# Performance work log

Measured on AMD Instinct MI355X. Metric: run time of the kernel, lower is better.

Reference implementation:

```python
import jax, jax.numpy as jnp
import numpy as np

B, S, D_IN, D_OUT = 8, 2048, 1024, 1024

def setup_inputs() -> dict:
    key = jax.random.key(0)
    ks = jax.random.split(key, 6)
    return {
        "inputs_for_keys": jax.random.normal(ks[0], (B, S, D_IN), dtype=jnp.float32),
        "inputs_for_values": jax.random.normal(ks[1], (B, S, D_IN), dtype=jnp.float32),
        "inputs_for_queries": jax.random.normal(ks[2], (B, S, D_IN), dtype=jnp.float32),
        "W_K": jax.random.normal(ks[3], (D_IN, D_OUT), dtype=jnp.float32) * 0.05,
        "W_V": jax.random.normal(ks[4], (D_IN, D_OUT), dtype=jnp.float32) * 0.05,
        "W_Q": jax.random.normal(ks[5], (D_IN, D_OUT), dtype=jnp.float32) * 0.05,
    }

def reference(inputs_for_keys, inputs_for_values, inputs_for_queries, W_K, W_V, W_Q):
    # Linear projections: [B,S,D_in] @ [D_in,D_out] -> [B,S,D_out]
    K = jnp.einsum("bsd,de->bse", inputs_for_keys, W_K)
    V = jnp.einsum("bsd,de->bse", inputs_for_values, W_V)
    Q = jnp.einsum("bsd,de->bse", inputs_for_queries, W_Q)
    scale = jnp.sqrt(jnp.asarray(K.shape[-1], dtype=K.dtype))
    # Scaled dot-product attention scores: [B,Sq,Sk]
    scores = jnp.einsum("bqe,bke->bqk", Q, K) / scale
    probs = jax.nn.softmax(scores, axis=-1)
    Z = jnp.einsum("bqk,bke->bqe", probs, V)
    return Z
```

## Files before the change

kernel.cpp:

```cpp
#include <hip/hip_runtime.h>
#include <hip/hip_bf16.h>
#include <stdint.h>

#define BATCH 8
#define SEQ 2048
#define DMODEL 1024

typedef __attribute__((ext_vector_type(4))) float f32x4;
typedef __attribute__((ext_vector_type(8))) short bf16x8;
typedef __attribute__((ext_vector_type(4))) uint32_t u32x4;
typedef __attribute__((ext_vector_type(2))) uint32_t u32x2;

#define MFMA16(a, b, c) __builtin_amdgcn_mfma_f32_16x16x32_bf16((a), (b), (c), 0, 0, 0)


static __device__ __forceinline__ uint16_t f2bf(float f) {
    uint32_t u = __builtin_bit_cast(uint32_t, f);
    u += 0x7fffu + ((u >> 16) & 1u);
    return (uint16_t)(u >> 16);
}
static __device__ __forceinline__ uint32_t pk2(float lo, float hi) {
    return (uint32_t)f2bf(lo) | ((uint32_t)f2bf(hi) << 16);
}
static __device__ __forceinline__ void gload16(const uint16_t* g, uint16_t* l) {
    __builtin_amdgcn_global_load_lds((const __attribute__((address_space(1))) void*)g,
                                     (__attribute__((address_space(3))) void*)l, 16, 0, 0);
}

__global__ __launch_bounds__(256) void cast_bf16_pk(const float* __restrict__ src,
                                                    uint16_t* __restrict__ dst) {
    const size_t c = (size_t)blockIdx.x * 256 + threadIdx.x;
    const size_t panel = c >> 11;
    const int w = (int)(c & 2047);
    const int ks = w >> 4, r15 = w & 15;
    const float* s = src + (panel * 16 + r15) * DMODEL + ks * 8;
    f32x4 a = *(const f32x4*)s;
    f32x4 b = *(const f32x4*)(s + 4);
    u32x4 o = {pk2(a[0], a[1]), pk2(a[2], a[3]), pk2(b[0], b[1]), pk2(b[2], b[3])};
    *(u32x4*)(dst + c * 8) = o;
}

__global__ void wt_cast_kernel(const float* __restrict__ Wk, const float* __restrict__ Wv,
                               const float* __restrict__ Wq, uint16_t* __restrict__ WT) {
    const float* W = blockIdx.z == 0 ? Wk : (blockIdx.z == 1 ? Wv : Wq);
    uint16_t* dst = WT + (size_t)blockIdx.z * DMODEL * DMODEL;
    __shared__ float tile[32][33];
    const int x = blockIdx.x * 32, y = blockIdx.y * 32;
    const int tx = threadIdx.x, ty = threadIdx.y;
#pragma unroll
    for (int j = 0; j < 4; j++)
        tile[ty * 4 + j][tx] = W[(size_t)(y + ty * 4 + j) * DMODEL + x + tx];
    __syncthreads();
#pragma unroll
    for (int j = 0; j < 4; j++) {
        const int n = x + ty * 4 + j, k = y + tx;
        const size_t off = ((size_t)(n >> 4) * (DMODEL / 8) + (k >> 3)) * 128 +
                           (n & 15) * 8 + (k & 7);
        dst[off] = f2bf(tile[tx][ty * 4 + j]);
    }
}

#define STAGE(tile, s)                                        \
    do {                                                      \
        const size_t ko_ = (size_t)(tile) * 512;              \
        gload16(Ab + ko_ + abase0, &As[s][t * 8]);            \
        gload16(Ab + ko_ + abase1, &As[s][t * 8 + 4096]);     \
        gload16(Bb + ko_ + bbase0, &Bs[s][t * 8]);            \
        gload16(Bb + ko_ + bbase1, &Bs[s][t * 8 + 4096]);     \
    } while (0)

#define KBODY(s, WAITSTR)                                                              \
    do {                                                                               \
        asm volatile("s_waitcnt " WAITSTR ::: "memory");                               \
        __builtin_amdgcn_s_barrier();                                                  \
        bf16x8 bfr[4], afr[8];                                                         \
        _Pragma("unroll") for (int j = 0; j < 4; j++)                                  \
            bfr[j] = *(const bf16x8*)&Bs[s][(wc * 4 + j) * 512 + lg * 128 + lr * 8];   \
        _Pragma("unroll") for (int i = 0; i < 8; i++)                                  \
            afr[i] = *(const bf16x8*)&As[s][(wr * 8 + i) * 512 + lg * 128 + lr * 8];   \
        __builtin_amdgcn_s_setprio(1);                                                 \
        _Pragma("unroll") for (int i = 0; i < 4; i++)                                  \
            _Pragma("unroll") for (int j = 0; j < 4; j++)                              \
                acc[i][j] = MFMA16(afr[i], bfr[j], acc[i][j]);                         \
        __builtin_amdgcn_s_setprio(0);                                                 \
        __builtin_amdgcn_s_setprio(1);                                                 \
        _Pragma("unroll") for (int i = 4; i < 8; i++)                                  \
            _Pragma("unroll") for (int j = 0; j < 4; j++)                              \
                acc[i][j] = MFMA16(afr[i], bfr[j], acc[i][j]);                         \
        __builtin_amdgcn_s_setprio(0);                                                 \
        asm volatile("s_waitcnt lgkmcnt(0)" ::: "memory");                             \
        __builtin_amdgcn_sched_barrier(0);                                             \
        __builtin_amdgcn_s_barrier();                                                  \
    } while (0)

template <int MODE, int BX>
__global__ __launch_bounds__(512, 2) void gemm256(const uint16_t* __restrict__ Ag,
                                                  const uint16_t* __restrict__ Bg,
                                                  void* __restrict__ Cg,
                                                  const float* __restrict__ Linv,
                                                  float scale, int lda, int ldb, int ldc,
                                                  int nk, size_t sA, size_t sB, size_t sC) {
    __shared__ __align__(16) uint16_t As[3][256 * 32];
    __shared__ __align__(16) uint16_t Bs[3][256 * 32];
    const int bz = BX ? blockIdx.x : blockIdx.z;
    const int bm = BX ? blockIdx.y : blockIdx.x;
    const int bn = BX ? blockIdx.z : blockIdx.y;
    const int m0 = bm * 256, n0 = bn * 256;
    const uint16_t* Ab = Ag + (size_t)bz * sA + (size_t)m0 * lda;
    const uint16_t* Bb = Bg + (size_t)bz * sB + (size_t)n0 * ldb;
    const int t = threadIdx.x, lane = t & 63;
    const int wid = t >> 6, wr = wid >> 2, wc = wid & 3;
    const int lr = lane & 15, lg = lane >> 4;
    const size_t eldA = (size_t)lda * 16, eldB = (size_t)ldb * 16;
    const size_t abase0 = (size_t)(t >> 6) * eldA + (t & 63) * 8;
    const size_t abase1 = abase0 + 8 * eldA;
    const size_t bbase0 = (size_t)(t >> 6) * eldB + (t & 63) * 8;
    const size_t bbase1 = bbase0 + 8 * eldB;

    f32x4 acc[8][4] = {};
    STAGE(0, 0);
    STAGE(1, 1);
    int s = 0, s2 = 2;
    for (int kt = 0; kt < nk - 2; ++kt) {
        STAGE(kt + 2, s2);
        KBODY(s, "vmcnt(8)");
        s = (s == 2) ? 0 : s + 1;
        s2 = (s2 == 2) ? 0 : s2 + 1;
    }
    KBODY(s, "vmcnt(4)");
    s = (s == 2) ? 0 : s + 1;
    KBODY(s, "vmcnt(0)");

    if constexpr (MODE == 0) {
        uint16_t* C = (uint16_t*)Cg + (size_t)bz * sC;
#pragma unroll
        for (int i = 0; i < 8; i++) {
            const int gm = m0 + wr * 128 + i * 16 + lg * 4;
            const size_t pbase = (size_t)(gm >> 4) * (ldc / 8);
#pragma unroll
            for (int j = 0; j < 4; j++) {
                const int gn = n0 + wc * 64 + j * 16 + lr;
                const size_t off = (pbase + (gn >> 3)) * 128 + (gn & 7);
#pragma unroll
                for (int r = 0; r < 4; r++)
                    C[off + (lg * 4 + r) * 8] = f2bf(acc[i][j][r] * scale);
            }
        }
    } else if constexpr (MODE == 1) {
        uint16_t* C = (uint16_t*)Cg;
#pragma unroll
        for (int i = 0; i < 8; i++) {
            const int gm = m0 + wr * 128 + i * 16 + lg * 4;
            const int bb = gm / SEQ;
            const int s0 = gm - bb * SEQ;
            uint16_t* Cb = C + (size_t)bb * DMODEL * SEQ;
#pragma unroll
            for (int j = 0; j < 4; j++) {
                const int e = n0 + wc * 64 + j * 16 + lr;
                const size_t off = ((size_t)(e >> 4) * (SEQ / 8) + (s0 >> 3)) * 128 +
                                   (e & 15) * 8 + (s0 & 7);
                u32x2 v = {pk2(acc[i][j][0], acc[i][j][1]), pk2(acc[i][j][2], acc[i][j][3])};
                *(u32x2*)&Cb[off] = v;
            }
        }
    } else {
        float* C = (float*)Cg + (size_t)bz * sC;
        const float* LB = Linv + bz * SEQ;
#pragma unroll
        for (int i = 0; i < 8; i++) {
            const int gm = m0 + wr * 128 + i * 16 + lg * 4;
            const f32x4 lv = *(const f32x4*)&LB[gm];
#pragma unroll
            for (int j = 0; j < 4; j++) {
                const int gn = n0 + wc * 64 + j * 16 + lr;
#pragma unroll
                for (int r = 0; r < 4; r++)
                    C[(size_t)(gm + r) * ldc + gn] = acc[i][j][r] * lv[r];
            }
        }
    }
}

__global__ __launch_bounds__(256) void softmax_pk(uint16_t* __restrict__ S,
                                                  float* __restrict__ Linv) {
    const size_t panel = blockIdx.x;
    uint16_t* sp = S + panel * (size_t)(16 * SEQ);
    const int t = threadIdx.x, lane = t & 63, w = t >> 6;
    const int r15 = t & 15, ksl = t >> 4;
    __shared__ float rm[4][16], rs[4][16];
    u32x4 raw[16];
    float mx = -3.0e38f;
#pragma unroll
    for (int u = 0; u < 16; u++) {
        raw[u] = *(const u32x4*)&sp[(ksl + u * 16) * 128 + r15 * 8];
#pragma unroll
        for (int j = 0; j < 4; j++) {
            mx = fmaxf(mx, __builtin_bit_cast(float, raw[u][j] << 16));
            mx = fmaxf(mx, __builtin_bit_cast(float, raw[u][j] & 0xffff0000u));
        }
    }
    mx = fmaxf(mx, __shfl_xor(mx, 16));
    mx = fmaxf(mx, __shfl_xor(mx, 32));
    if (lane < 16) rm[w][lane] = mx;
    __syncthreads();
    const float m = fmaxf(fmaxf(rm[0][r15], rm[1][r15]), fmaxf(rm[2][r15], rm[3][r15]));
    float sum = 0.0f;
#pragma unroll
    for (int u = 0; u < 16; u++) {
#pragma unroll
        for (int j = 0; j < 4; j++) {
            float lo = __expf(__builtin_bit_cast(float, raw[u][j] << 16) - m);
            float hi = __expf(__builtin_bit_cast(float, raw[u][j] & 0xffff0000u) - m);
            sum += lo + hi;
            raw[u][j] = pk2(lo, hi);
        }
    }
    sum += __shfl_xor(sum, 16);
    sum += __shfl_xor(sum, 32);
    if (lane < 16) rs[w][lane] = sum;
    __syncthreads();
    const float tot = rs[0][r15] + rs[1][r15] + rs[2][r15] + rs[3][r15];
#pragma unroll
    for (int u = 0; u < 16; u++)
        *(u32x4*)&sp[(ksl + u * 16) * 128 + r15 * 8] = raw[u];
    if (w == 0 && lane < 16) Linv[panel * 16 + lane] = 1.0f / tot;
}

extern "C" void kernel_launch(void* const* d_in, const int* in_sizes, int n_in,
                              void* d_out, int out_size, void* d_ws, size_t ws_size,
                              hipStream_t stream) {
    const float* Xk = (const float*)d_in[0];
    const float* Xv = (const float*)d_in[1];
    const float* Xq = (const float*)d_in[2];
    const float* Wk = (const float*)d_in[3];
    const float* Wv = (const float*)d_in[4];
    const float* Wq = (const float*)d_in[5];
    float* out = (float*)d_out;
    char* ws = (char*)d_ws;
    uint16_t* Qbf = (uint16_t*)(ws);
    uint16_t* Kbf = (uint16_t*)(ws + (size_t)33554432);
    uint16_t* VTb = (uint16_t*)(ws + (size_t)67108864);
    uint16_t* WT  = (uint16_t*)(ws + (size_t)100663296);
    float*    Linv= (float*)(ws + (size_t)106954752);
    uint16_t* Sb  = (uint16_t*)(ws + (size_t)107020288);
    uint16_t* Xbf = (uint16_t*)(ws + (size_t)171966464);

    wt_cast_kernel<<<dim3(32, 32, 3), dim3(32, 8), 0, stream>>>(Wk, Wv, Wq, WT);
    cast_bf16_pk<<<8192, 256, 0, stream>>>(Xq, Xbf);
    gemm256<0, 0><<<dim3(64, 4, 1), 512, 0, stream>>>(
        Xbf, WT + 2 * 1048576, (void*)Qbf, nullptr, 0.03125f,
        DMODEL, DMODEL, DMODEL, DMODEL / 32, 0, 0, 0);
    cast_bf16_pk<<<8192, 256, 0, stream>>>(Xk, Xbf);
    gemm256<0, 0><<<dim3(64, 4, 1), 512, 0, stream>>>(
        Xbf, WT, (void*)Kbf, nullptr, 1.0f,
        DMODEL, DMODEL, DMODEL, DMODEL / 32, 0, 0, 0);
    cast_bf16_pk<<<8192, 256, 0, stream>>>(Xv, Xbf);
    gemm256<1, 0><<<dim3(64, 4, 1), 512, 0, stream>>>(
        Xbf, WT + 1048576, (void*)VTb, nullptr, 1.0f,
        DMODEL, DMODEL, 0, DMODEL / 32, 0, 0, 0);
    gemm256<0, 1><<<dim3(8, 8, 8), 512, 0, stream>>>(
        Qbf, Kbf, (void*)Sb, nullptr, 1.0f,
        DMODEL, DMODEL, SEQ, DMODEL / 32,
        (size_t)SEQ * DMODEL, (size_t)SEQ * DMODEL, (size_t)SEQ * SEQ);
    softmax_pk<<<dim3(BATCH * SEQ / 16), 256, 0, stream>>>(Sb, Linv);
    gemm256<2, 1><<<dim3(8, 8, 4), 512, 0, stream>>>(
        Sb, VTb, (void*)out, Linv, 1.0f,
        SEQ, SEQ, DMODEL, SEQ / 32,
        (size_t)SEQ * SEQ, (size_t)DMODEL * SEQ, (size_t)SEQ * DMODEL);
}
```

Measured before the change: 405.7 us.

## Parameterize GEMM N-tile width and switch to double-buffered LDS pipeline

```diff
diff --git a/kernel.cpp b/kernel.cpp
--- a/kernel.cpp
+++ b/kernel.cpp
@@ -60,32 +60,33 @@
     }
 }
 
-#define STAGE(tile, s)                                        \
-    do {                                                      \
-        const size_t ko_ = (size_t)(tile) * 512;              \
-        gload16(Ab + ko_ + abase0, &As[s][t * 8]);            \
-        gload16(Ab + ko_ + abase1, &As[s][t * 8 + 4096]);     \
-        gload16(Bb + ko_ + bbase0, &Bs[s][t * 8]);            \
-        gload16(Bb + ko_ + bbase1, &Bs[s][t * 8 + 4096]);     \
+#define STAGE(tile, s)                                                       \
+    do {                                                                     \
+        const size_t ko_ = (size_t)(tile) * 512;                             \
+        gload16(Ab + ko_ + abase0, &As[s][t * 8]);                           \
+        gload16(Ab + ko_ + abase1, &As[s][t * 8 + 4096]);                    \
+        gload16(Bb + ko_ + bbase0, &Bs[s][t * 8]);                           \
+        if constexpr (NB == 4)                                               \
+            gload16(Bb + ko_ + bbase1, &Bs[s][t * 8 + 4096]);                \
     } while (0)
 
 #define KBODY(s, WAITSTR)                                                              \
     do {                                                                               \
         asm volatile("s_waitcnt " WAITSTR ::: "memory");                               \
         __builtin_amdgcn_s_barrier();                                                  \
-        bf16x8 bfr[4], afr[8];                                                         \
-        _Pragma("unroll") for (int j = 0; j < 4; j++)                                  \
-            bfr[j] = *(const bf16x8*)&Bs[s][(wc * 4 + j) * 512 + lg * 128 + lr * 8];   \
+        bf16x8 bfr[NB], afr[8];                                                        \
+        _Pragma("unroll") for (int j = 0; j < NB; j++)                                 \
+            bfr[j] = *(const bf16x8*)&Bs[s][(wc * NB + j) * 512 + lg * 128 + lr * 8];  \
         _Pragma("unroll") for (int i = 0; i < 8; i++)                                  \
             afr[i] = *(const bf16x8*)&As[s][(wr * 8 + i) * 512 + lg * 128 + lr * 8];   \
         __builtin_amdgcn_s_setprio(1);                                                 \
         _Pragma("unroll") for (int i = 0; i < 4; i++)                                  \
-            _Pragma("unroll") for (int j = 0; j < 4; j++)                              \
+            _Pragma("unroll") for (int j = 0; j < NB; j++)                             \
                 acc[i][j] = MFMA16(afr[i], bfr[j], acc[i][j]);                         \
         __builtin_amdgcn_s_setprio(0);                                                 \
         __builtin_amdgcn_s_setprio(1);                                                 \
         _Pragma("unroll") for (int i = 4; i < 8; i++)                                  \
-            _Pragma("unroll") for (int j = 0; j < 4; j++)                              \
+            _Pragma("unroll") for (int j = 0; j < NB; j++)                             \
                 acc[i][j] = MFMA16(afr[i], bfr[j], acc[i][j]);                         \
         __builtin_amdgcn_s_setprio(0);                                                 \
         asm volatile("s_waitcnt lgkmcnt(0)" ::: "memory");                             \
@@ -93,19 +94,19 @@
         __builtin_amdgcn_s_barrier();                                                  \
     } while (0)
 
-template <int MODE, int BX>
+template <int MODE, int BX, int NB>
 __global__ __launch_bounds__(512, 2) void gemm256(const uint16_t* __restrict__ Ag,
                                                   const uint16_t* __restrict__ Bg,
                                                   void* __restrict__ Cg,
                                                   const float* __restrict__ Linv,
                                                   float scale, int lda, int ldb, int ldc,
                                                   int nk, size_t sA, size_t sB, size_t sC) {
-    __shared__ __align__(16) uint16_t As[3][256 * 32];
-    __shared__ __align__(16) uint16_t Bs[3][256 * 32];
+    __shared__ __align__(16) uint16_t As[2][256 * 32];
+    __shared__ __align__(16) uint16_t Bs[2][NB * 64 * 32];
     const int bz = BX ? blockIdx.x : blockIdx.z;
     const int bm = BX ? blockIdx.y : blockIdx.x;
     const int bn = BX ? blockIdx.z : blockIdx.y;
-    const int m0 = bm * 256, n0 = bn * 256;
+    const int m0 = bm * 256, n0 = bn * (NB * 64);
     const uint16_t* Ab = Ag + (size_t)bz * sA + (size_t)m0 * lda;
     const uint16_t* Bb = Bg + (size_t)bz * sB + (size_t)n0 * ldb;
     const int t = threadIdx.x, lane = t & 63;
@@ -117,19 +118,19 @@
     const size_t bbase0 = (size_t)(t >> 6) * eldB + (t & 63) * 8;
     const size_t bbase1 = bbase0 + 8 * eldB;
 
-    f32x4 acc[8][4] = {};
+    f32x4 acc[8][NB] = {};
     STAGE(0, 0);
-    STAGE(1, 1);
-    int s = 0, s2 = 2;
-    for (int kt = 0; kt < nk - 2; ++kt) {
-        STAGE(kt + 2, s2);
-        KBODY(s, "vmcnt(8)");
-        s = (s == 2) ? 0 : s + 1;
-        s2 = (s2 == 2) ? 0 : s2 + 1;
-    }
-    KBODY(s, "vmcnt(4)");
-    s = (s == 2) ? 0 : s + 1;
-    KBODY(s, "vmcnt(0)");
+    int buf = 0;
+    for (int kt = 0; kt < nk; ++kt) {
+        if (kt + 1 < nk) {
+            STAGE(kt + 1, buf ^ 1);
+            if constexpr (NB == 4) { KBODY(buf, "vmcnt(4)"); }
+            else                   { KBODY(buf, "vmcnt(3)"); }
+        } else {
+            KBODY(buf, "vmcnt(0)");
+        }
+        buf ^= 1;
+    }
 
     if constexpr (MODE == 0) {
         uint16_t* C = (uint16_t*)Cg + (size_t)bz * sC;
@@ -138,8 +139,8 @@
             const int gm = m0 + wr * 128 + i * 16 + lg * 4;
             const size_t pbase = (size_t)(gm >> 4) * (ldc / 8);
 #pragma unroll
-            for (int j = 0; j < 4; j++) {
-                const int gn = n0 + wc * 64 + j * 16 + lr;
+            for (int j = 0; j < NB; j++) {
+                const int gn = n0 + wc * (NB * 16) + j * 16 + lr;
                 const size_t off = (pbase + (gn >> 3)) * 128 + (gn & 7);
 #pragma unroll
                 for (int r = 0; r < 4; r++)
@@ -155,8 +156,8 @@
             const int s0 = gm - bb * SEQ;
             uint16_t* Cb = C + (size_t)bb * DMODEL * SEQ;
 #pragma unroll
-            for (int j = 0; j < 4; j++) {
-                const int e = n0 + wc * 64 + j * 16 + lr;
+            for (int j = 0; j < NB; j++) {
+                const int e = n0 + wc * (NB * 16) + j * 16 + lr;
                 const size_t off = ((size_t)(e >> 4) * (SEQ / 8) + (s0 >> 3)) * 128 +
                                    (e & 15) * 8 + (s0 & 7);
                 u32x2 v = {pk2(acc[i][j][0], acc[i][j][1]), pk2(acc[i][j][2], acc[i][j][3])};
@@ -171,8 +172,8 @@
             const int gm = m0 + wr * 128 + i * 16 + lg * 4;
             const f32x4 lv = *(const f32x4*)&LB[gm];
 #pragma unroll
-            for (int j = 0; j < 4; j++) {
-                const int gn = n0 + wc * 64 + j * 16 + lr;
+            for (int j = 0; j < NB; j++) {
+                const int gn = n0 + wc * (NB * 16) + j * 16 + lr;
 #pragma unroll
                 for (int r = 0; r < 4; r++)
                     C[(size_t)(gm + r) * ldc + gn] = acc[i][j][r] * lv[r];
@@ -247,23 +248,23 @@
 
     wt_cast_kernel<<<dim3(32, 32, 3), dim3(32, 8), 0, stream>>>(Wk, Wv, Wq, WT);
     cast_bf16_pk<<<8192, 256, 0, stream>>>(Xq, Xbf);
-    gemm256<0, 0><<<dim3(64, 4, 1), 512, 0, stream>>>(
+    gemm256<0, 0, 2><<<dim3(64, 8, 1), 512, 0, stream>>>(
         Xbf, WT + 2 * 1048576, (void*)Qbf, nullptr, 0.03125f,
         DMODEL, DMODEL, DMODEL, DMODEL / 32, 0, 0, 0);
     cast_bf16_pk<<<8192, 256, 0, stream>>>(Xk, Xbf);
-    gemm256<0, 0><<<dim3(64, 4, 1), 512, 0, stream>>>(
+    gemm256<0, 0, 2><<<dim3(64, 8, 1), 512, 0, stream>>>(
         Xbf, WT, (void*)Kbf, nullptr, 1.0f,
         DMODEL, DMODEL, DMODEL, DMODEL / 32, 0, 0, 0);
     cast_bf16_pk<<<8192, 256, 0, stream>>>(Xv, Xbf);
-    gemm256<1, 0><<<dim3(64, 4, 1), 512, 0, stream>>>(
+    gemm256<1, 0, 2><<<dim3(64, 8, 1), 512, 0, stream>>>(
         Xbf, WT + 1048576, (void*)VTb, nullptr, 1.0f,
         DMODEL, DMODEL, 0, DMODEL / 32, 0, 0, 0);
-    gemm256<0, 1><<<dim3(8, 8, 8), 512, 0, stream>>>(
+    gemm256<0, 1, 4><<<dim3(8, 8, 8), 512, 0, stream>>>(
         Qbf, Kbf, (void*)Sb, nullptr, 1.0f,
         DMODEL, DMODEL, SEQ, DMODEL / 32,
         (size_t)SEQ * DMODEL, (size_t)SEQ * DMODEL, (size_t)SEQ * SEQ);
     softmax_pk<<<dim3(BATCH * SEQ / 16), 256, 0, stream>>>(Sb, Linv);
-    gemm256<2, 1><<<dim3(8, 8, 4), 512, 0, stream>>>(
+    gemm256<2, 1, 2><<<dim3(8, 8, 8), 512, 0, stream>>>(
         Sb, VTb, (void*)out, Linv, 1.0f,
         SEQ, SEQ, DMODEL, SEQ / 32,
         (size_t)SEQ * SEQ, (size_t)DMODEL * SEQ, (size_t)SEQ * DMODEL);
```

New measurement: 825.3 us. 103% more time.

## Restructure GEMM main loop into 8-phase ping-pong with 64-wide K tiles

Applied to the files above, without the earlier changes.

```diff
diff --git a/kernel.cpp b/kernel.cpp
--- a/kernel.cpp
+++ b/kernel.cpp
@@ -60,76 +60,105 @@
     }
 }
 
-#define STAGE(tile, s)                                        \
-    do {                                                      \
-        const size_t ko_ = (size_t)(tile) * 512;              \
-        gload16(Ab + ko_ + abase0, &As[s][t * 8]);            \
-        gload16(Ab + ko_ + abase1, &As[s][t * 8 + 4096]);     \
-        gload16(Bb + ko_ + bbase0, &Bs[s][t * 8]);            \
-        gload16(Bb + ko_ + bbase1, &Bs[s][t * 8 + 4096]);     \
+#define STG_A(kt, sl, h)                                                          \
+    do {                                                                          \
+        const size_t g0 = (size_t)((h) * 8 + (tid >> 7)) * eldA +                 \
+                          (size_t)(kt) * 1024 + (tid & 127) * 8;                  \
+        gload16(Ab + g0, &As[sl][(h) * 8192 + tid * 8]);                          \
+        gload16(Ab + g0 + 4 * eldA, &As[sl][(h) * 8192 + tid * 8 + 4096]);        \
     } while (0)
-
-#define KBODY(s, WAITSTR)                                                              \
-    do {                                                                               \
-        asm volatile("s_waitcnt " WAITSTR ::: "memory");                               \
-        __builtin_amdgcn_s_barrier();                                                  \
-        bf16x8 bfr[4], afr[8];                                                         \
-        _Pragma("unroll") for (int j = 0; j < 4; j++)                                  \
-            bfr[j] = *(const bf16x8*)&Bs[s][(wc * 4 + j) * 512 + lg * 128 + lr * 8];   \
-        _Pragma("unroll") for (int i = 0; i < 8; i++)                                  \
-            afr[i] = *(const bf16x8*)&As[s][(wr * 8 + i) * 512 + lg * 128 + lr * 8];   \
-        __builtin_amdgcn_s_setprio(1);                                                 \
-        _Pragma("unroll") for (int i = 0; i < 4; i++)                                  \
-            _Pragma("unroll") for (int j = 0; j < 4; j++)                              \
-                acc[i][j] = MFMA16(afr[i], bfr[j], acc[i][j]);                         \
-        __builtin_amdgcn_s_setprio(0);                                                 \
-        __builtin_amdgcn_s_setprio(1);                                                 \
-        _Pragma("unroll") for (int i = 4; i < 8; i++)                                  \
-            _Pragma("unroll") for (int j = 0; j < 4; j++)                              \
-                acc[i][j] = MFMA16(afr[i], bfr[j], acc[i][j]);                         \
-        __builtin_amdgcn_s_setprio(0);                                                 \
-        asm volatile("s_waitcnt lgkmcnt(0)" ::: "memory");                             \
-        __builtin_amdgcn_sched_barrier(0);                                             \
-        __builtin_amdgcn_s_barrier();                                                  \
+#define STG_B(kt, sl, h)                                                          \
+    do {                                                                          \
+        const size_t g0 = (size_t)((h) * 8 + (tid >> 7)) * eldB +                 \
+                          (size_t)(kt) * 1024 + (tid & 127) * 8;                  \
+        gload16(Bb + g0, &Bs[sl][(h) * 8192 + tid * 8]);                          \
+        gload16(Bb + g0 + 4 * eldB, &Bs[sl][(h) * 8192 + tid * 8 + 4096]);        \
     } while (0)
 
+#define READ_B(sl)                                                                \
+    _Pragma("unroll") for (int j = 0; j < 4; j++) {                               \
+        bfr[j][0] = *(const bf16x8*)&Bs[sl][(wc * 4 + j) * 1024 + lbase];         \
+        bfr[j][1] = *(const bf16x8*)&Bs[sl][(wc * 4 + j) * 1024 + 512 + lbase];   \
+    }
+
+#define VM4 asm volatile("s_waitcnt vmcnt(4)" ::: "memory")
+#define VM0 asm volatile("s_waitcnt vmcnt(0)" ::: "memory")
+#define NOPW (void)0
+#define NOST (void)0
+
+#define PH(sl, q, STG, WAIT)                                                      \
+    do {                                                                          \
+        const int ab = (wr * 8 + 2 * (q)) * 1024 + lbase;                         \
+        bf16x8 a00 = *(const bf16x8*)&As[sl][ab];                                 \
+        bf16x8 a01 = *(const bf16x8*)&As[sl][ab + 512];                           \
+        bf16x8 a10 = *(const bf16x8*)&As[sl][ab + 1024];                          \
+        bf16x8 a11 = *(const bf16x8*)&As[sl][ab + 1536];                          \
+        STG;                                                                      \
+        WAIT;                                                                     \
+        __builtin_amdgcn_s_barrier();                                             \
+        asm volatile("s_waitcnt lgkmcnt(0)" ::: "memory");                        \
+        __builtin_amdgcn_sched_barrier(0);                                        \
+        __builtin_amdgcn_s_setprio(1);                                            \
+        _Pragma("unroll") for (int j = 0; j < 4; j++) {                           \
+            acc[2 * (q)][j] = MFMA16(a00, bfr[j][0], acc[2 * (q)][j]);            \
+            acc[2 * (q)][j] = MFMA16(a01, bfr[j][1], acc[2 * (q)][j]);            \
+            acc[2 * (q) + 1][j] = MFMA16(a10, bfr[j][0], acc[2 * (q) + 1][j]);    \
+            acc[2 * (q) + 1][j] = MFMA16(a11, bfr[j][1], acc[2 * (q) + 1][j]);    \
+        }                                                                         \
+        __builtin_amdgcn_s_setprio(0);                                            \
+        __builtin_amdgcn_s_barrier();                                             \
+    } while (0)
+
 template <int MODE, int BX>
-__global__ __launch_bounds__(512, 2) void gemm256(const uint16_t* __restrict__ Ag,
-                                                  const uint16_t* __restrict__ Bg,
-                                                  void* __restrict__ Cg,
-                                                  const float* __restrict__ Linv,
-                                                  float scale, int lda, int ldb, int ldc,
-                                                  int nk, size_t sA, size_t sB, size_t sC) {
-    __shared__ __align__(16) uint16_t As[3][256 * 32];
-    __shared__ __align__(16) uint16_t Bs[3][256 * 32];
+__global__ __launch_bounds__(512, 2) void gemm8p(const uint16_t* __restrict__ Ag,
+                                                 const uint16_t* __restrict__ Bg,
+                                                 void* __restrict__ Cg,
+                                                 const float* __restrict__ Linv,
+                                                 float scale, int lda, int ldb, int ldc,
+                                                 int nk, size_t sA, size_t sB, size_t sC) {
+    __shared__ __align__(16) uint16_t As[2][16384];
+    __shared__ __align__(16) uint16_t Bs[2][16384];
     const int bz = BX ? blockIdx.x : blockIdx.z;
     const int bm = BX ? blockIdx.y : blockIdx.x;
     const int bn = BX ? blockIdx.z : blockIdx.y;
     const int m0 = bm * 256, n0 = bn * 256;
     const uint16_t* Ab = Ag + (size_t)bz * sA + (size_t)m0 * lda;
     const uint16_t* Bb = Bg + (size_t)bz * sB + (size_t)n0 * ldb;
-    const int t = threadIdx.x, lane = t & 63;
-    const int wid = t >> 6, wr = wid >> 2, wc = wid & 3;
+    const int tid = threadIdx.x, lane = tid & 63;
+    const int wid = tid >> 6, wr = wid >> 2, wc = wid & 3;
     const int lr = lane & 15, lg = lane >> 4;
+    const int lbase = lg * 128 + lr * 8;
     const size_t eldA = (size_t)lda * 16, eldB = (size_t)ldb * 16;
-    const size_t abase0 = (size_t)(t >> 6) * eldA + (t & 63) * 8;
-    const size_t abase1 = abase0 + 8 * eldA;
-    const size_t bbase0 = (size_t)(t >> 6) * eldB + (t & 63) * 8;
-    const size_t bbase1 = bbase0 + 8 * eldB;
 
     f32x4 acc[8][4] = {};
-    STAGE(0, 0);
-    STAGE(1, 1);
-    int s = 0, s2 = 2;
-    for (int kt = 0; kt < nk - 2; ++kt) {
-        STAGE(kt + 2, s2);
-        KBODY(s, "vmcnt(8)");
-        s = (s == 2) ? 0 : s + 1;
-        s2 = (s2 == 2) ? 0 : s2 + 1;
-    }
-    KBODY(s, "vmcnt(4)");
-    s = (s == 2) ? 0 : s + 1;
-    KBODY(s, "vmcnt(0)");
+    bf16x8 bfr[4][2];
+    STG_A(0, 0, 0); STG_A(0, 0, 1);
+    STG_B(0, 0, 0); STG_B(0, 0, 1);
+    STG_B(1, 1, 0); STG_B(1, 1, 1);
+    VM4;
+    __builtin_amdgcn_s_barrier();
+    for (int kt = 0; kt + 3 < nk; kt += 2) {
+        READ_B(0);
+        PH(0, 0, STG_A(kt + 1, 1, 0), NOPW);
+        PH(0, 1, STG_A(kt + 1, 1, 1), NOPW);
+        PH(0, 2, STG_B(kt + 2, 0, 0), NOPW);
+        PH(0, 3, STG_B(kt + 2, 0, 1), VM4);
+        READ_B(1);
+        PH(1, 0, STG_A(kt + 2, 0, 0), NOPW);
+        PH(1, 1, STG_A(kt + 2, 0, 1), NOPW);
+        PH(1, 2, STG_B(kt + 3, 1, 0), NOPW);
+        PH(1, 3, STG_B(kt + 3, 1, 1), VM4);
+    }
+    READ_B(0);
+    PH(0, 0, STG_A(nk - 1, 1, 0), NOPW);
+    PH(0, 1, STG_A(nk - 1, 1, 1), NOPW);
+    PH(0, 2, NOST, NOPW);
+    PH(0, 3, NOST, VM0);
+    READ_B(1);
+    PH(1, 0, NOST, NOPW);
+    PH(1, 1, NOST, NOPW);
+    PH(1, 2, NOST, NOPW);
+    PH(1, 3, NOST, NOPW);
 
     if constexpr (MODE == 0) {
         uint16_t* C = (uint16_t*)Cg + (size_t)bz * sC;
@@ -247,24 +276,24 @@
 
     wt_cast_kernel<<<dim3(32, 32, 3), dim3(32, 8), 0, stream>>>(Wk, Wv, Wq, WT);
     cast_bf16_pk<<<8192, 256, 0, stream>>>(Xq, Xbf);
-    gemm256<0, 0><<<dim3(64, 4, 1), 512, 0, stream>>>(
+    gemm8p<0, 0><<<dim3(64, 4, 1), 512, 0, stream>>>(
         Xbf, WT + 2 * 1048576, (void*)Qbf, nullptr, 0.03125f,
-        DMODEL, DMODEL, DMODEL, DMODEL / 32, 0, 0, 0);
+        DMODEL, DMODEL, DMODEL, DMODEL / 64, 0, 0, 0);
     cast_bf16_pk<<<8192, 256, 0, stream>>>(Xk, Xbf);
-    gemm256<0, 0><<<dim3(64, 4, 1), 512, 0, stream>>>(
+    gemm8p<0, 0><<<dim3(64, 4, 1), 512, 0, stream>>>(
         Xbf, WT, (void*)Kbf, nullptr, 1.0f,
-        DMODEL, DMODEL, DMODEL, DMODEL / 32, 0, 0, 0);
+        DMODEL, DMODEL, DMODEL, DMODEL / 64, 0, 0, 0);
     cast_bf16_pk<<<8192, 256, 0, stream>>>(Xv, Xbf);
-    gemm256<1, 0><<<dim3(64, 4, 1), 512, 0, stream>>>(
+    gemm8p<1, 0><<<dim3(64, 4, 1), 512, 0, stream>>>(
         Xbf, WT + 1048576, (void*)VTb, nullptr, 1.0f,
-        DMODEL, DMODEL, 0, DMODEL / 32, 0, 0, 0);
-    gemm256<0, 1><<<dim3(8, 8, 8), 512, 0, stream>>>(
+        DMODEL, DMODEL, 0, DMODEL / 64, 0, 0, 0);
+    gemm8p<0, 1><<<dim3(8, 8, 8), 512, 0, stream>>>(
         Qbf, Kbf, (void*)Sb, nullptr, 1.0f,
-        DMODEL, DMODEL, SEQ, DMODEL / 32,
+        DMODEL, DMODEL, SEQ, DMODEL / 64,
         (size_t)SEQ * DMODEL, (size_t)SEQ * DMODEL, (size_t)SEQ * SEQ);
     softmax_pk<<<dim3(BATCH * SEQ / 16), 256, 0, stream>>>(Sb, Linv);
-    gemm256<2, 1><<<dim3(8, 8, 4), 512, 0, stream>>>(
+    gemm8p<2, 1><<<dim3(8, 8, 4), 512, 0, stream>>>(
         Sb, VTb, (void*)out, Linv, 1.0f,
-        SEQ, SEQ, DMODEL, SEQ / 32,
+        SEQ, SEQ, DMODEL, SEQ / 64,
         (size_t)SEQ * SEQ, (size_t)DMODEL * SEQ, (size_t)SEQ * DMODEL);
 }
```

Measured after the change: 369.7 us. 1.1x faster.
